# Kernel optimization log

Measured on AMD Instinct MI355X. Metric: run time of the kernel, lower is better.

The kernel has to match this reference:

```python
import jax, jax.numpy as jnp
import numpy as np

B, S, D, H = 2, 2048, 1024, 16
HD = D // H  # 64


def setup_inputs() -> dict:
    key = jax.random.key(0)
    ks = jax.random.split(key, 10)
    s = 1.0 / np.sqrt(D)
    X = jax.random.normal(ks[0], (B, S, D), dtype=jnp.float32)
    # pad the last 256 key positions (nonzero = ignore); causal rows still
    # attend to earlier unpadded keys so no all-masked rows.
    kpm = jnp.broadcast_to((jnp.arange(S) >= S - 256).astype(jnp.int32), (B, S))
    return {
        "X": X,
        "key_padding_mask": kpm,
        "Wq": jax.random.uniform(ks[1], (D, D), jnp.float32, -s, s),
        "bq": jax.random.uniform(ks[2], (D,), jnp.float32, -s, s),
        "Wk": jax.random.uniform(ks[3], (D, D), jnp.float32, -s, s),
        "bk": jax.random.uniform(ks[4], (D,), jnp.float32, -s, s),
        "Wv": jax.random.uniform(ks[5], (D, D), jnp.float32, -s, s),
        "bv": jax.random.uniform(ks[6], (D,), jnp.float32, -s, s),
        "Wo": jax.random.uniform(ks[7], (D, D), jnp.float32, -s, s),
        "bo": jax.random.uniform(ks[8], (D,), jnp.float32, -s, s),
    }


def _mha(X, kpm, Wq, bq, Wk, bk, Wv, bv, Wo, bo):
    b, s, d = X.shape
    def heads(t):  # (b,s,d) -> (b,H,s,hd)
        return t.reshape(b, s, H, HD).transpose(0, 2, 1, 3)
    Q = heads(X @ Wq.T + bq)
    K = heads(X @ Wk.T + bk)
    V = heads(X @ Wv.T + bv)
    scores = jnp.einsum('bhqd,bhkd->bhqk', Q, K) / jnp.sqrt(jnp.float32(HD))
    causal = jnp.triu(jnp.ones((s, s), dtype=bool), k=1)  # True above diag
    scores = jnp.where(causal[None, None], -jnp.inf, scores)
    scores = jnp.where(kpm[:, None, None, :] != 0, -jnp.inf, scores)
    A = jax.nn.softmax(scores, axis=-1)
    out = jnp.einsum('bhqk,bhkd->bhqd', A, V)  # (b,H,s,hd)
    out = out.transpose(0, 2, 1, 3).reshape(b, s, d)
    return out @ Wo.T + bo


def reference(X, key_padding_mask, Wq, bq, Wk, bk, Wv, bv, Wo, bo):
    return _mha(X, key_padding_mask, Wq, bq, Wk, bk, Wv, bv, Wo, bo)
```

## Files before the change

### kernel.cpp

```cpp
#include <hip/hip_runtime.h>
#include <math.h>

#define DEV __device__ __forceinline__

typedef __attribute__((ext_vector_type(4))) float f32x4;
typedef __attribute__((ext_vector_type(8))) __bf16 bf16x8;

static constexpr int Bc = 2, Sc = 2048, Dc = 1024, Hc = 16, HDc = 64;
static constexpr int LDQ = 3 * Dc;
static constexpr float SCL = 0.125f * 1.44269504f;

DEV unsigned short f2b(float f) {
  union { float f; unsigned int u; } c; c.f = f;
  unsigned int u = c.u;
  unsigned int r = (u + 0x7fffu + ((u >> 16) & 1u)) >> 16;
  return (unsigned short)r;
}

DEV void async16(const void* g, void* l) {
  __builtin_amdgcn_global_load_lds(
      (__attribute__((address_space(1))) void*)(void*)g,
      (__attribute__((address_space(3))) void*)l, 16, 0, 0);
}

DEV int swz(int r, int c) { return r * 64 + (c ^ ((r & 7) << 3)); }

__global__ void cvt_x(const float* __restrict__ in,
                      unsigned short* __restrict__ out, int n4) {
  int i = blockIdx.x * blockDim.x + threadIdx.x;
  if (i < n4) {
    const float4 v = reinterpret_cast<const float4*>(in)[i];
    ushort4 o;
    o.x = f2b(v.x); o.y = f2b(v.y); o.z = f2b(v.z); o.w = f2b(v.w);
    reinterpret_cast<ushort4*>(out)[i] = o;
  }
}

__global__ void cvt_w(const float* __restrict__ w0, const float* __restrict__ w1,
                      const float* __restrict__ w2, const float* __restrict__ w3,
                      unsigned short* __restrict__ out) {
  const float* src = blockIdx.y == 0 ? w0
                     : blockIdx.y == 1 ? w1
                     : blockIdx.y == 2 ? w2 : w3;
  const int i = blockIdx.x * blockDim.x + threadIdx.x;
  const float4 v = reinterpret_cast<const float4*>(src)[i];
  ushort4 o;
  o.x = f2b(v.x); o.y = f2b(v.y); o.z = f2b(v.z); o.w = f2b(v.w);
  reinterpret_cast<ushort4*>(out)[(size_t)blockIdx.y * (Dc * Dc / 4) + i] = o;
}

template <typename OUT>
__global__ __launch_bounds__(256, 3) void gemm_bt(
    const unsigned short* __restrict__ A, const unsigned short* __restrict__ Bm,
    const float* __restrict__ b0, const float* __restrict__ b1,
    const float* __restrict__ b2, OUT* __restrict__ C, int M, int K, int ldc) {
  __shared__ unsigned short As[128 * 64];
  __shared__ unsigned short Bs[128 * 64];
  const int tid = threadIdx.x;
  const int wave = tid >> 6, lane = tid & 63;
  const int wr = wave >> 1, wc = wave & 1;
  const int cpx = gridDim.x >> 3;
  const int swzid = (blockIdx.x & 7) * cpx + (blockIdx.x >> 3);
  const int row0 = (swzid & 31) * 128, col0 = (swzid >> 5) * 128;
  const int srow = lane >> 3, scol = (lane & 7) * 8;

  f32x4 acc[4][4];
#pragma unroll
  for (int m = 0; m < 4; ++m)
#pragma unroll
    for (int n = 0; n < 4; ++n) acc[m][n] = {0.f, 0.f, 0.f, 0.f};

  for (int k0 = 0; k0 < K; k0 += 64) {
    __syncthreads();
#pragma unroll
    for (int c = 0; c < 4; ++c) {
      const int rr = (wave * 4 + c) * 8 + srow;
      async16(A + (size_t)(row0 + rr) * K + k0 + scol,
              (char*)As + (wave * 4 + c) * 1024);
      async16(Bm + (size_t)(col0 + rr) * K + k0 + scol,
              (char*)Bs + (wave * 4 + c) * 1024);
    }
    __syncthreads();
#pragma unroll
    for (int ks = 0; ks < 2; ++ks) {
      const int kk = ks * 32 + (lane >> 4) * 8;
      bf16x8 af[4], bfr[4];
#pragma unroll
      for (int m = 0; m < 4; ++m)
        af[m] = *reinterpret_cast<const bf16x8*>(
            &As[(wr * 64 + m * 16 + (lane & 15)) * 64 + kk]);
#pragma unroll
      for (int n = 0; n < 4; ++n)
        bfr[n] = *reinterpret_cast<const bf16x8*>(
            &Bs[(wc * 64 + n * 16 + (lane & 15)) * 64 + kk]);
#pragma unroll
      for (int m = 0; m < 4; ++m)
#pragma unroll
        for (int n = 0; n < 4; ++n)
          acc[m][n] = __builtin_amdgcn_mfma_f32_16x16x32_bf16(af[m], bfr[n],
                                                              acc[m][n], 0, 0, 0);
    }
  }
  const int r4 = (lane >> 4) * 4, cl = lane & 15;
#pragma unroll
  for (int n = 0; n < 4; ++n) {
    const int gc = col0 + wc * 64 + n * 16 + cl;
    const float* bp = gc < Dc ? b0 : (gc < 2 * Dc ? b1 : b2);
    const float bv = bp[gc & (Dc - 1)];
#pragma unroll
    for (int m = 0; m < 4; ++m) {
#pragma unroll
      for (int j = 0; j < 4; ++j) {
        const int gr = row0 + wr * 64 + m * 16 + r4 + j;
        const float v = acc[m][n][j] + bv;
        if constexpr (sizeof(OUT) == 4)
          C[(size_t)gr * ldc + gc] = v;
        else
          C[(size_t)gr * ldc + gc] = (OUT)f2b(v);
      }
    }
  }
}

__global__ __launch_bounds__(256, 4) void attn_fwd(
    const __bf16* __restrict__ Qg, const __bf16* __restrict__ Kg,
    const __bf16* __restrict__ Vg, const int* __restrict__ kpm,
    __bf16* __restrict__ Og) {
  __shared__ __bf16 QP[64 * 64];
  __shared__ __bf16 Ks[2][64 * 64];
  __shared__ __bf16 Vt[2][64 * 64];

  const int L = blockIdx.x;
  const int s = L >> 8, c = L & 255;
  const int u = c >> 5, bh = c & 31;
  const int qb = s * 8 + ((s & 1) ? (7 - u) : u);

  const int b = bh >> 4, h = bh & 15;
  const int q0 = qb * 64;
  const int tid = threadIdx.x, wave = tid >> 6, lane = tid & 63;
  const size_t base = (size_t)b * Sc * LDQ + (size_t)h * HDc;
  const int srow = lane >> 3;
  const int scol = 8 * ((lane & 7) ^ srow);
  const int hi = lane >> 4, cl = lane & 15, r4 = hi * 4;

  const int vk2 = (tid & 31) * 2, vd8 = (tid >> 5) * 8;
  const __bf16* vbase = Vg + base + (size_t)vk2 * LDQ + vd8;
  const int* mbase = kpm + b * Sc;

  union VV { uint4 q; unsigned short u[8]; };

#pragma unroll
  for (int cc = 0; cc < 2; ++cc) {
    const int rr = (wave * 2 + cc) * 8 + srow;
    async16(Qg + base + (size_t)(q0 + rr) * LDQ + scol,
            (char*)QP + (wave * 2 + cc) * 1024);
    async16(Kg + base + (size_t)rr * LDQ + scol,
            (char*)Ks[0] + (wave * 2 + cc) * 1024);
  }
  VV v0, v1;
  v0.q = *reinterpret_cast<const uint4*>(vbase);
  v1.q = *reinterpret_cast<const uint4*>(vbase + LDQ);
  int mki[4];
#pragma unroll
  for (int n = 0; n < 4; ++n) mki[n] = mbase[n * 16 + cl];
  {
    unsigned int* V32 = reinterpret_cast<unsigned int*>(Vt[0]);
#pragma unroll
    for (int i = 0; i < 8; ++i) {
      const int row = vd8 + i;
      V32[row * 32 + ((tid & 31) ^ ((row & 7) << 2))] =
          (unsigned int)v0.u[i] | ((unsigned int)v1.u[i] << 16);
    }
  }
  __syncthreads();

  bf16x8 qf[2];
#pragma unroll
  for (int ks = 0; ks < 2; ++ks)
    qf[ks] = *reinterpret_cast<const bf16x8*>(
        &QP[swz(wave * 16 + cl, ks * 32 + hi * 8)]);
  __bf16* Ps = QP + wave * 1024;

  bf16x8 ones;
#pragma unroll
  for (int i = 0; i < 8; ++i) ones[i] = (__bf16)1.0f;

  f32x4 o[4], lacc;
  float m_[4];
#pragma unroll
  for (int n = 0; n < 4; ++n) o[n] = {0.f, 0.f, 0.f, 0.f};
  lacc = {0.f, 0.f, 0.f, 0.f};
#pragma unroll
  for (int j = 0; j < 4; ++j) m_[j] = -1e30f;

  int pb = 0;
  for (int kb = 0; kb <= qb; ++kb) {
    const bool diag = (kb == qb);
    VV n0, n1;
    int nmk[4];
    if (!diag) {
      const int k1 = (kb + 1) * 64;
#pragma unroll
      for (int cc = 0; cc < 2; ++cc) {
        const int rr = (wave * 2 + cc) * 8 + srow;
        async16(Kg + base + (size_t)(k1 + rr) * LDQ + scol,
                (char*)Ks[pb ^ 1] + (wave * 2 + cc) * 1024);
      }
      n0.q = *reinterpret_cast<const uint4*>(vbase + (size_t)k1 * LDQ);
      n1.q = *reinterpret_cast<const uint4*>(vbase + (size_t)(k1 + 1) * LDQ);
#pragma unroll
      for (int n = 0; n < 4; ++n) nmk[n] = mbase[k1 + n * 16 + cl];
    }

    f32x4 sa[4];
#pragma unroll
    for (int n = 0; n < 4; ++n) sa[n] = {0.f, 0.f, 0.f, 0.f};
    __builtin_amdgcn_s_setprio(1);
#pragma unroll
    for (int ks = 0; ks < 2; ++ks) {
      const int kk = ks * 32 + hi * 8;
#pragma unroll
      for (int n = 0; n < 4; ++n) {
        if (!(diag && n > wave)) {
          const bf16x8 kf = *reinterpret_cast<const bf16x8*>(
              &Ks[pb][swz(n * 16 + cl, kk)]);
          sa[n] = __builtin_amdgcn_mfma_f32_16x16x32_bf16(qf[ks], kf, sa[n],
                                                          0, 0, 0);
        }
      }
    }
    __builtin_amdgcn_s_setprio(0);
    float pm[4] = {-1e30f, -1e30f, -1e30f, -1e30f};
#pragma unroll
    for (int n = 0; n < 4; ++n) {
      const float mf = mki[n] ? -1e30f : 0.0f;
#pragma unroll
      for (int j = 0; j < 4; ++j) {
        float s2 = fmaf(sa[n][j], SCL, mf);
        if (diag && (kb * 64 + n * 16 + cl > q0 + wave * 16 + r4 + j))
          s2 = -1e30f;
        sa[n][j] = s2;
        pm[j] = fmaxf(pm[j], s2);
      }
    }
    const bool ok = (pm[0] - m_[0] <= 8.f) && (pm[1] - m_[1] <= 8.f) &&
                    (pm[2] - m_[2] <= 8.f) && (pm[3] - m_[3] <= 8.f);
    if (!__all(ok)) {
#pragma unroll
      for (int off = 1; off < 16; off <<= 1)
#pragma unroll
        for (int j = 0; j < 4; ++j)
          pm[j] = fmaxf(pm[j], __shfl_xor(pm[j], off, 64));
#pragma unroll
      for (int j = 0; j < 4; ++j) {
        const float mn = fmaxf(m_[j], pm[j]);
        const float sc = __builtin_amdgcn_exp2f(m_[j] - mn);
        m_[j] = mn;
        lacc[j] *= sc;
#pragma unroll
        for (int n = 0; n < 4; ++n) o[n][j] *= sc;
      }
    }
#pragma unroll
    for (int n = 0; n < 4; ++n)
#pragma unroll
      for (int j = 0; j < 4; ++j) {
        const float p = __builtin_amdgcn_exp2f(sa[n][j] - m_[j]);
        Ps[swz(r4 + j, n * 16 + cl)] = (__bf16)p;
      }
    __builtin_amdgcn_s_setprio(1);
#pragma unroll
    for (int ks = 0; ks < 2; ++ks) {
      const int kk = ks * 32 + hi * 8;
      const bf16x8 pf = *reinterpret_cast<const bf16x8*>(&Ps[swz(cl, kk)]);
#pragma unroll
      for (int n = 0; n < 4; ++n) {
        const bf16x8 vf = *reinterpret_cast<const bf16x8*>(
            &Vt[pb][swz(n * 16 + cl, kk)]);
        o[n] = __builtin_amdgcn_mfma_f32_16x16x32_bf16(pf, vf, o[n], 0, 0, 0);
      }
      lacc = __builtin_amdgcn_mfma_f32_16x16x32_bf16(pf, ones, lacc, 0, 0, 0);
    }
    __builtin_amdgcn_s_setprio(0);
    if (!diag) {
      unsigned int* V32 = reinterpret_cast<unsigned int*>(Vt[pb ^ 1]);
#pragma unroll
      for (int i = 0; i < 8; ++i) {
        const int row = vd8 + i;
        V32[row * 32 + ((tid & 31) ^ ((row & 7) << 2))] =
            (unsigned int)n0.u[i] | ((unsigned int)n1.u[i] << 16);
      }
#pragma unroll
      for (int n = 0; n < 4; ++n) mki[n] = nmk[n];
    }
    __syncthreads();
    pb ^= 1;
  }

#pragma unroll
  for (int j = 0; j < 4; ++j) {
    const float inv = 1.f / lacc[j];
#pragma unroll
    for (int n = 0; n < 4; ++n)
      Og[(size_t)(b * Sc + q0 + wave * 16 + r4 + j) * Dc + h * HDc + n * 16 +
         cl] = (__bf16)(o[n][j] * inv);
  }
}

extern "C" void kernel_launch(void* const* d_in, const int* in_sizes, int n_in,
                              void* d_out, int out_size, void* d_ws,
                              size_t ws_size, hipStream_t stream) {
  const float* X = (const float*)d_in[0];
  const int* kpm = (const int*)d_in[1];
  const float* Wq = (const float*)d_in[2];
  const float* bq = (const float*)d_in[3];
  const float* Wk = (const float*)d_in[4];
  const float* bk = (const float*)d_in[5];
  const float* Wv = (const float*)d_in[6];
  const float* bv = (const float*)d_in[7];
  const float* Wo = (const float*)d_in[8];
  const float* bo = (const float*)d_in[9];
  float* out = (float*)d_out;

  char* w = (char*)d_ws;
  unsigned short* Xb = (unsigned short*)(w);
  unsigned short* Wqkvb = (unsigned short*)(w + (8u << 20));
  unsigned short* Wob = (unsigned short*)(w + (14u << 20));
  unsigned short* QKVb = (unsigned short*)(w + (16u << 20));
  unsigned short* Ab = (unsigned short*)(w + (40u << 20));

  const int MD = Bc * Sc;
  cvt_x<<<dim3(MD * Dc / 1024), 256, 0, stream>>>(X, Xb, MD * Dc / 4);
  cvt_w<<<dim3(Dc * Dc / 1024, 4), 256, 0, stream>>>(Wq, Wk, Wv, Wo, Wqkvb);

  gemm_bt<unsigned short><<<dim3(32 * 24), 256, 0, stream>>>(
      Xb, Wqkvb, bq, bk, bv, QKVb, MD, Dc, LDQ);

  attn_fwd<<<dim3(1024), 256, 0, stream>>>(
      (const __bf16*)QKVb, (const __bf16*)QKVb + Dc,
      (const __bf16*)QKVb + 2 * Dc, kpm, (__bf16*)Ab);

  gemm_bt<float><<<dim3(32 * 8), 256, 0, stream>>>(
      Ab, Wob, bo, bo, bo, out, MD, Dc, Dc);
}
```

Measured before the change: 121.6 us.

## Split long causal attention rows across two KV chunks with a combine kernel

Query blocks 8..31 are split into two KV-range chunks, each processed by its own workgroup. Each chunk writes unnormalized bf16 partial outputs plus row max and sum to workspace. A new combine kernel merges the two chunks with log-sum-exp rescaling. The aim is to cut the long tail of the causal workload and even out per-block work, at the cost of an extra launch, partial-result traffic and bf16 rounding of the partials.

```diff
diff --git a/kernel.cpp b/kernel.cpp
--- a/kernel.cpp
+++ b/kernel.cpp
@@ -125,18 +125,36 @@
 __global__ __launch_bounds__(256, 4) void attn_fwd(
     const __bf16* __restrict__ Qg, const __bf16* __restrict__ Kg,
     const __bf16* __restrict__ Vg, const int* __restrict__ kpm,
-    __bf16* __restrict__ Og) {
+    __bf16* __restrict__ Og, __bf16* __restrict__ OP,
+    float* __restrict__ ML) {
   __shared__ __bf16 QP[64 * 64];
   __shared__ __bf16 Ks[2][64 * 64];
   __shared__ __bf16 Vt[2][64 * 64];
 
   const int L = blockIdx.x;
-  const int s = L >> 8, c = L & 255;
-  const int u = c >> 5, bh = c & 31;
-  const int qb = s * 8 + ((s & 1) ? (7 - u) : u);
+  int bh, qb, kb0, kb1, pidx;
+  bool split;
+  if (L < 1536) {
+    qb = 31 - (L >> 6);
+    const int chunk = (L >> 5) & 1;
+    bh = L & 31;
+    const int c0 = (qb + 1) >> 1;
+    kb0 = chunk ? c0 : 0;
+    kb1 = chunk ? qb : c0 - 1;
+    split = true;
+    pidx = (bh * 24 + (qb - 8)) * 2 + chunk;
+  } else {
+    const int b2 = L - 1536;
+    qb = 7 - (b2 >> 5);
+    bh = b2 & 31;
+    kb0 = 0; kb1 = qb;
+    split = false;
+    pidx = 0;
+  }
 
   const int b = bh >> 4, h = bh & 15;
   const int q0 = qb * 64;
+  const int k00 = kb0 * 64;
   const int tid = threadIdx.x, wave = tid >> 6, lane = tid & 63;
   const size_t base = (size_t)b * Sc * LDQ + (size_t)h * HDc;
   const int srow = lane >> 3;
@@ -154,15 +172,15 @@
     const int rr = (wave * 2 + cc) * 8 + srow;
     async16(Qg + base + (size_t)(q0 + rr) * LDQ + scol,
             (char*)QP + (wave * 2 + cc) * 1024);
-    async16(Kg + base + (size_t)rr * LDQ + scol,
+    async16(Kg + base + (size_t)(k00 + rr) * LDQ + scol,
             (char*)Ks[0] + (wave * 2 + cc) * 1024);
   }
   VV v0, v1;
-  v0.q = *reinterpret_cast<const uint4*>(vbase);
-  v1.q = *reinterpret_cast<const uint4*>(vbase + LDQ);
+  v0.q = *reinterpret_cast<const uint4*>(vbase + (size_t)k00 * LDQ);
+  v1.q = *reinterpret_cast<const uint4*>(vbase + (size_t)(k00 + 1) * LDQ);
   int mki[4];
 #pragma unroll
-  for (int n = 0; n < 4; ++n) mki[n] = mbase[n * 16 + cl];
+  for (int n = 0; n < 4; ++n) mki[n] = mbase[k00 + n * 16 + cl];
   {
     unsigned int* V32 = reinterpret_cast<unsigned int*>(Vt[0]);
 #pragma unroll
@@ -194,11 +212,12 @@
   for (int j = 0; j < 4; ++j) m_[j] = -1e30f;
 
   int pb = 0;
-  for (int kb = 0; kb <= qb; ++kb) {
+  for (int kb = kb0; kb <= kb1; ++kb) {
+    const bool last = (kb == kb1);
     const bool diag = (kb == qb);
     VV n0, n1;
     int nmk[4];
-    if (!diag) {
+    if (!last) {
       const int k1 = (kb + 1) * 64;
 #pragma unroll
       for (int cc = 0; cc < 2; ++cc) {
@@ -282,7 +301,7 @@
       lacc = __builtin_amdgcn_mfma_f32_16x16x32_bf16(pf, ones, lacc, 0, 0, 0);
     }
     __builtin_amdgcn_s_setprio(0);
-    if (!diag) {
+    if (!last) {
       unsigned int* V32 = reinterpret_cast<unsigned int*>(Vt[pb ^ 1]);
 #pragma unroll
       for (int i = 0; i < 8; ++i) {
@@ -297,14 +316,64 @@
     pb ^= 1;
   }
 
-#pragma unroll
-  for (int j = 0; j < 4; ++j) {
-    const float inv = 1.f / lacc[j];
-#pragma unroll
-    for (int n = 0; n < 4; ++n)
-      Og[(size_t)(b * Sc + q0 + wave * 16 + r4 + j) * Dc + h * HDc + n * 16 +
-         cl] = (__bf16)(o[n][j] * inv);
-  }
+  if (!split) {
+#pragma unroll
+    for (int j = 0; j < 4; ++j) {
+      const float inv = 1.f / lacc[j];
+#pragma unroll
+      for (int n = 0; n < 4; ++n)
+        Og[(size_t)(b * Sc + q0 + wave * 16 + r4 + j) * Dc + h * HDc + n * 16 +
+           cl] = (__bf16)(o[n][j] * inv);
+    }
+  } else {
+    __bf16* op = OP + (size_t)pidx * 4096;
+    float* ml = ML + (size_t)pidx * 128;
+#pragma unroll
+    for (int j = 0; j < 4; ++j) {
+      const int row = wave * 16 + r4 + j;
+      if (cl == 0) {
+        ml[row * 2 + 0] = m_[j];
+        ml[row * 2 + 1] = lacc[j];
+      }
+#pragma unroll
+      for (int n = 0; n < 4; ++n) op[row * 64 + n * 16 + cl] = (__bf16)o[n][j];
+    }
+  }
+}
+
+__global__ __launch_bounds__(256) void attn_combine(
+    const __bf16* __restrict__ OP, const float* __restrict__ ML,
+    __bf16* __restrict__ Og) {
+  const int qq = blockIdx.x;
+  const int bh = blockIdx.y;
+  const int qb = 8 + qq;
+  const int b = bh >> 4, h = bh & 15;
+  const int t = threadIdx.x;
+  const int row = t >> 2, c0 = (t & 3) * 16;
+  const int p0 = (bh * 24 + qq) * 2;
+  const __bf16* o1 = OP + (size_t)p0 * 4096 + row * 64 + c0;
+  const __bf16* o2 = OP + (size_t)(p0 + 1) * 4096 + row * 64 + c0;
+  const float m1 = ML[(size_t)p0 * 128 + row * 2];
+  const float l1 = ML[(size_t)p0 * 128 + row * 2 + 1];
+  const float m2 = ML[(size_t)(p0 + 1) * 128 + row * 2];
+  const float l2 = ML[(size_t)(p0 + 1) * 128 + row * 2 + 1];
+  const float m = fmaxf(m1, m2);
+  const float s1 = __builtin_amdgcn_exp2f(m1 - m);
+  const float s2 = __builtin_amdgcn_exp2f(m2 - m);
+  const float inv = 1.f / (l1 * s1 + l2 * s2);
+  const bf16x8 a0 = *reinterpret_cast<const bf16x8*>(o1);
+  const bf16x8 a1 = *reinterpret_cast<const bf16x8*>(o1 + 8);
+  const bf16x8 b0 = *reinterpret_cast<const bf16x8*>(o2);
+  const bf16x8 b1 = *reinterpret_cast<const bf16x8*>(o2 + 8);
+  bf16x8 r0, r1;
+#pragma unroll
+  for (int i = 0; i < 8; ++i) {
+    r0[i] = (__bf16)(((float)a0[i] * s1 + (float)b0[i] * s2) * inv);
+    r1[i] = (__bf16)(((float)a1[i] * s1 + (float)b1[i] * s2) * inv);
+  }
+  __bf16* dst = Og + (size_t)(b * Sc + qb * 64 + row) * Dc + h * HDc + c0;
+  *reinterpret_cast<bf16x8*>(dst) = r0;
+  *reinterpret_cast<bf16x8*>(dst + 8) = r1;
 }
 
 extern "C" void kernel_launch(void* const* d_in, const int* in_sizes, int n_in,
@@ -328,6 +397,8 @@
   unsigned short* Wob = (unsigned short*)(w + (14u << 20));
   unsigned short* QKVb = (unsigned short*)(w + (16u << 20));
   unsigned short* Ab = (unsigned short*)(w + (40u << 20));
+  __bf16* OP = (__bf16*)(w);
+  float* ML = (float*)(w + 12'582'912);
 
   const int MD = Bc * Sc;
   cvt_x<<<dim3(MD * Dc / 1024), 256, 0, stream>>>(X, Xb, MD * Dc / 4);
@@ -336,9 +407,10 @@
   gemm_bt<unsigned short><<<dim3(32 * 24), 256, 0, stream>>>(
       Xb, Wqkvb, bq, bk, bv, QKVb, MD, Dc, LDQ);
 
-  attn_fwd<<<dim3(1024), 256, 0, stream>>>(
+  attn_fwd<<<dim3(1792), 256, 0, stream>>>(
       (const __bf16*)QKVb, (const __bf16*)QKVb + Dc,
-      (const __bf16*)QKVb + 2 * Dc, kpm, (__bf16*)Ab);
+      (const __bf16*)QKVb + 2 * Dc, kpm, (__bf16*)Ab, OP, ML);
+  attn_combine<<<dim3(24, 32), 256, 0, stream>>>(OP, ML, (__bf16*)Ab);
 
   gemm_bt<float><<<dim3(32 * 8), 256, 0, stream>>>(
       Ab, Wob, bo, bo, bo, out, MD, Dc, Dc);
```

Result: slower. 129.1 us (+6.2%).

## Use 256x256 double-buffered QKV GEMM and merge conversion kernels

Applied to the files above, without the earlier changes.

Replaces the 128x128 QKV projection GEMM with a new 512-thread kernel using 256x256 tiles, double-buffered async global-to-LDS loads, split barriers and raised wave priority around the MFMA block. The larger tile raises arithmetic intensity and cuts global traffic per FLOP. The X and weight bf16 conversion kernels are merged into one launch to save launch overhead. Risks: only 192 blocks for 256 CUs, so some CUs sit idle and occupancy drops, and the epilogue stores scalar bf16 values.

```diff
diff --git a/kernel.cpp b/kernel.cpp
--- a/kernel.cpp
+++ b/kernel.cpp
@@ -25,28 +25,138 @@
 
 DEV int swz(int r, int c) { return r * 64 + (c ^ ((r & 7) << 3)); }
 
-__global__ void cvt_x(const float* __restrict__ in,
-                      unsigned short* __restrict__ out, int n4) {
-  int i = blockIdx.x * blockDim.x + threadIdx.x;
-  if (i < n4) {
-    const float4 v = reinterpret_cast<const float4*>(in)[i];
-    ushort4 o;
-    o.x = f2b(v.x); o.y = f2b(v.y); o.z = f2b(v.z); o.w = f2b(v.w);
-    reinterpret_cast<ushort4*>(out)[i] = o;
-  }
-}
-
-__global__ void cvt_w(const float* __restrict__ w0, const float* __restrict__ w1,
-                      const float* __restrict__ w2, const float* __restrict__ w3,
-                      unsigned short* __restrict__ out) {
-  const float* src = blockIdx.y == 0 ? w0
-                     : blockIdx.y == 1 ? w1
-                     : blockIdx.y == 2 ? w2 : w3;
+__global__ void cvt_all(const float* __restrict__ X, const float* __restrict__ Wq,
+                        const float* __restrict__ Wk, const float* __restrict__ Wv,
+                        const float* __restrict__ Wo,
+                        unsigned short* __restrict__ Xb,
+                        unsigned short* __restrict__ Wb) {
   const int i = blockIdx.x * blockDim.x + threadIdx.x;
-  const float4 v = reinterpret_cast<const float4*>(src)[i];
-  ushort4 o;
-  o.x = f2b(v.x); o.y = f2b(v.y); o.z = f2b(v.z); o.w = f2b(v.w);
-  reinterpret_cast<ushort4*>(out)[(size_t)blockIdx.y * (Dc * Dc / 4) + i] = o;
+  const float* src;
+  unsigned short* dst;
+  int o;
+  if (i < (1 << 20)) {
+    src = X; o = i; dst = Xb;
+  } else {
+    const int wi = i - (1 << 20);
+    const int m = wi >> 18;
+    src = m == 0 ? Wq : m == 1 ? Wk : m == 2 ? Wv : Wo;
+    o = wi & ((1 << 18) - 1);
+    dst = Wb + (size_t)m * (Dc * Dc);
+  }
+  const float4 v = reinterpret_cast<const float4*>(src)[o];
+  ushort4 u;
+  u.x = f2b(v.x); u.y = f2b(v.y); u.z = f2b(v.z); u.w = f2b(v.w);
+  reinterpret_cast<ushort4*>(dst)[o] = u;
+}
+
+__global__ __launch_bounds__(512, 2) void gemm256(
+    const unsigned short* __restrict__ A, const unsigned short* __restrict__ Bm,
+    const float* __restrict__ b0, const float* __restrict__ b1,
+    const float* __restrict__ b2, unsigned short* __restrict__ C, int K,
+    int ldc) {
+  __shared__ unsigned short As2[2][256 * 64];
+  __shared__ unsigned short Bs2[2][256 * 64];
+  const int tid = threadIdx.x;
+  const int wave = tid >> 6, lane = tid & 63;
+  const int wr = wave >> 2, wc = wave & 3;
+  const int hi = lane >> 4, cl = lane & 15;
+  const int L = K / 64 - 1;
+
+  const int cpx = gridDim.x >> 3;
+  const int id = (blockIdx.x & 7) * cpx + (blockIdx.x >> 3);
+  const int row0 = (id / 12) * 256, col0 = (id % 12) * 256;
+
+  const int trow = tid >> 3;
+  const int scolw = 8 * ((tid & 7) ^ (trow & 7));
+  const unsigned short* Abase = A + (size_t)(row0 + trow) * K + scolw;
+  const unsigned short* Bbase = Bm + (size_t)(col0 + trow) * K + scolw;
+
+  auto stA = [&](int kt, int h) {
+#pragma unroll
+    for (int c = 0; c < 2; ++c)
+      async16(Abase + (size_t)(h * 128 + c * 64) * K + kt * 64,
+              (char*)&As2[kt & 1][(h * 128 + c * 64 + wave * 8) * 64] +
+                  lane * 16);
+  };
+  auto stB = [&](int kt, int h) {
+#pragma unroll
+    for (int c = 0; c < 2; ++c)
+      async16(Bbase + (size_t)(h * 128 + c * 64) * K + kt * 64,
+              (char*)&Bs2[kt & 1][(h * 128 + c * 64 + wave * 8) * 64] +
+                  lane * 16);
+  };
+
+  f32x4 acc[8][4];
+#pragma unroll
+  for (int m = 0; m < 8; ++m)
+#pragma unroll
+    for (int n = 0; n < 4; ++n) acc[m][n] = {0.f, 0.f, 0.f, 0.f};
+
+  stB(0, 0); stB(0, 1); stA(0, 0); stA(0, 1); stB(1, 0); stB(1, 1);
+
+  for (int kt = 0; kt <= L; ++kt) {
+    const int d = kt & 1;
+    if (kt < L)
+      asm volatile("s_waitcnt vmcnt(4)" ::: "memory");
+    else
+      asm volatile("s_waitcnt vmcnt(0)" ::: "memory");
+    __builtin_amdgcn_s_barrier();
+    __builtin_amdgcn_sched_barrier(0);
+
+    bf16x8 bfr[4][2];
+#pragma unroll
+    for (int n = 0; n < 4; ++n)
+#pragma unroll
+      for (int ks = 0; ks < 2; ++ks)
+        bfr[n][ks] = *reinterpret_cast<const bf16x8*>(
+            &Bs2[d][swz(wc * 64 + n * 16 + cl, ks * 32 + hi * 8)]);
+
+#pragma unroll
+    for (int p = 0; p < 4; ++p) {
+      if (p == 2) {
+        __builtin_amdgcn_s_barrier();
+        __builtin_amdgcn_sched_barrier(0);
+      }
+      if (p == 0 && kt < L) stA(kt + 1, 0);
+      if (p == 1 && kt < L) stA(kt + 1, 1);
+      if (p == 2 && kt < L - 1) stB(kt + 2, 0);
+      if (p == 3 && kt < L - 1) stB(kt + 2, 1);
+
+      bf16x8 af[2][2];
+#pragma unroll
+      for (int mf = 0; mf < 2; ++mf)
+#pragma unroll
+        for (int ks = 0; ks < 2; ++ks)
+          af[mf][ks] = *reinterpret_cast<const bf16x8*>(
+              &As2[d][swz(wr * 128 + p * 32 + mf * 16 + cl,
+                          ks * 32 + hi * 8)]);
+      __builtin_amdgcn_s_setprio(1);
+#pragma unroll
+      for (int mf = 0; mf < 2; ++mf)
+#pragma unroll
+        for (int n = 0; n < 4; ++n)
+#pragma unroll
+          for (int ks = 0; ks < 2; ++ks)
+            acc[p * 2 + mf][n] = __builtin_amdgcn_mfma_f32_16x16x32_bf16(
+                af[mf][ks], bfr[n][ks], acc[p * 2 + mf][n], 0, 0, 0);
+      __builtin_amdgcn_s_setprio(0);
+    }
+  }
+
+#pragma unroll
+  for (int n = 0; n < 4; ++n) {
+    const int gc = col0 + wc * 64 + n * 16 + cl;
+    const float* bp = gc < Dc ? b0 : (gc < 2 * Dc ? b1 : b2);
+    const float bv = bp[gc & (Dc - 1)];
+#pragma unroll
+    for (int m = 0; m < 8; ++m) {
+#pragma unroll
+      for (int j = 0; j < 4; ++j) {
+        const int gr = row0 + wr * 128 + m * 16 + hi * 4 + j;
+        C[(size_t)gr * ldc + gc] = f2b(acc[m][n][j] + bv);
+      }
+    }
+  }
 }
 
 template <typename OUT>
@@ -330,11 +440,9 @@
   unsigned short* Ab = (unsigned short*)(w + (40u << 20));
 
   const int MD = Bc * Sc;
-  cvt_x<<<dim3(MD * Dc / 1024), 256, 0, stream>>>(X, Xb, MD * Dc / 4);
-  cvt_w<<<dim3(Dc * Dc / 1024, 4), 256, 0, stream>>>(Wq, Wk, Wv, Wo, Wqkvb);
-
-  gemm_bt<unsigned short><<<dim3(32 * 24), 256, 0, stream>>>(
-      Xb, Wqkvb, bq, bk, bv, QKVb, MD, Dc, LDQ);
+  cvt_all<<<dim3(8192), 256, 0, stream>>>(X, Wq, Wk, Wv, Wo, Xb, Wqkvb);
+
+  gemm256<<<dim3(192), 512, 0, stream>>>(Xb, Wqkvb, bq, bk, bv, QKVb, Dc, LDQ);
 
   attn_fwd<<<dim3(1024), 256, 0, stream>>>(
       (const __bf16*)QKVb, (const __bf16*)QKVb + Dc,
```

After: 125.1 us. +2.9%, slower.

## Transpose QK^T MFMA so each lane owns one query row; fuse converts

Applied to the files above, without the earlier changes.

Swaps the MFMA operands for S=QK^T so each lane holds scores for a single query row, which lets the softmax row max be a scalar per lane reduced with two cross-lane shuffles instead of four-way vectors over 16 lanes. The key padding mask is precomputed once as additive float values, stored temporarily in the output buffer and loaded as f32x4. The X and weight conversion kernels are merged into one launch that also builds the mask. In exchange, the P tile is written to LDS in a transposed pattern and the rescale factor is broadcast with per-row shuffles, which may add LDS bank conflicts and shuffle cost.

```diff
diff --git a/kernel.cpp b/kernel.cpp
--- a/kernel.cpp
+++ b/kernel.cpp
@@ -25,28 +25,34 @@
 
 DEV int swz(int r, int c) { return r * 64 + (c ^ ((r & 7) << 3)); }
 
-__global__ void cvt_x(const float* __restrict__ in,
-                      unsigned short* __restrict__ out, int n4) {
-  int i = blockIdx.x * blockDim.x + threadIdx.x;
-  if (i < n4) {
-    const float4 v = reinterpret_cast<const float4*>(in)[i];
-    ushort4 o;
-    o.x = f2b(v.x); o.y = f2b(v.y); o.z = f2b(v.z); o.w = f2b(v.w);
-    reinterpret_cast<ushort4*>(out)[i] = o;
-  }
-}
-
-__global__ void cvt_w(const float* __restrict__ w0, const float* __restrict__ w1,
-                      const float* __restrict__ w2, const float* __restrict__ w3,
-                      unsigned short* __restrict__ out) {
-  const float* src = blockIdx.y == 0 ? w0
-                     : blockIdx.y == 1 ? w1
-                     : blockIdx.y == 2 ? w2 : w3;
+__global__ void cvt_all(const float* __restrict__ X, const float* __restrict__ Wq,
+                        const float* __restrict__ Wk, const float* __restrict__ Wv,
+                        const float* __restrict__ Wo, const int* __restrict__ kpm,
+                        unsigned short* __restrict__ Xb,
+                        unsigned short* __restrict__ Wb,
+                        float* __restrict__ mfl) {
   const int i = blockIdx.x * blockDim.x + threadIdx.x;
-  const float4 v = reinterpret_cast<const float4*>(src)[i];
-  ushort4 o;
-  o.x = f2b(v.x); o.y = f2b(v.y); o.z = f2b(v.z); o.w = f2b(v.w);
-  reinterpret_cast<ushort4*>(out)[(size_t)blockIdx.y * (Dc * Dc / 4) + i] = o;
+  if (i >= (1 << 21)) {
+    const int mi = i - (1 << 21);
+    if (mi < Bc * Sc) mfl[mi] = kpm[mi] ? -1e30f : 0.0f;
+    return;
+  }
+  const float* src;
+  unsigned short* dst;
+  int o;
+  if (i < (1 << 20)) {
+    src = X; o = i; dst = Xb;
+  } else {
+    const int wi = i - (1 << 20);
+    const int m = wi >> 18;
+    src = m == 0 ? Wq : m == 1 ? Wk : m == 2 ? Wv : Wo;
+    o = wi & ((1 << 18) - 1);
+    dst = Wb + (size_t)m * (Dc * Dc);
+  }
+  const float4 v = reinterpret_cast<const float4*>(src)[o];
+  ushort4 u;
+  u.x = f2b(v.x); u.y = f2b(v.y); u.z = f2b(v.z); u.w = f2b(v.w);
+  reinterpret_cast<ushort4*>(dst)[o] = u;
 }
 
 template <typename OUT>
@@ -124,7 +130,7 @@
 
 __global__ __launch_bounds__(256, 4) void attn_fwd(
     const __bf16* __restrict__ Qg, const __bf16* __restrict__ Kg,
-    const __bf16* __restrict__ Vg, const int* __restrict__ kpm,
+    const __bf16* __restrict__ Vg, const float* __restrict__ mfl,
     __bf16* __restrict__ Og) {
   __shared__ __bf16 QP[64 * 64];
   __shared__ __bf16 Ks[2][64 * 64];
@@ -142,10 +148,11 @@
   const int srow = lane >> 3;
   const int scol = 8 * ((lane & 7) ^ srow);
   const int hi = lane >> 4, cl = lane & 15, r4 = hi * 4;
+  const int myq = q0 + wave * 16 + cl;
 
   const int vk2 = (tid & 31) * 2, vd8 = (tid >> 5) * 8;
   const __bf16* vbase = Vg + base + (size_t)vk2 * LDQ + vd8;
-  const int* mbase = kpm + b * Sc;
+  const float* mbase = mfl + b * Sc;
 
   union VV { uint4 q; unsigned short u[8]; };
 
@@ -160,9 +167,10 @@
   VV v0, v1;
   v0.q = *reinterpret_cast<const uint4*>(vbase);
   v1.q = *reinterpret_cast<const uint4*>(vbase + LDQ);
-  int mki[4];
-#pragma unroll
-  for (int n = 0; n < 4; ++n) mki[n] = mbase[n * 16 + cl];
+  f32x4 mk[4];
+#pragma unroll
+  for (int n = 0; n < 4; ++n)
+    mk[n] = *reinterpret_cast<const f32x4*>(&mbase[n * 16 + hi * 4]);
   {
     unsigned int* V32 = reinterpret_cast<unsigned int*>(Vt[0]);
 #pragma unroll
@@ -186,18 +194,16 @@
   for (int i = 0; i < 8; ++i) ones[i] = (__bf16)1.0f;
 
   f32x4 o[4], lacc;
-  float m_[4];
+  float m_ = -1e30f;
 #pragma unroll
   for (int n = 0; n < 4; ++n) o[n] = {0.f, 0.f, 0.f, 0.f};
   lacc = {0.f, 0.f, 0.f, 0.f};
-#pragma unroll
-  for (int j = 0; j < 4; ++j) m_[j] = -1e30f;
 
   int pb = 0;
   for (int kb = 0; kb <= qb; ++kb) {
     const bool diag = (kb == qb);
     VV n0, n1;
-    int nmk[4];
+    f32x4 nmk[4];
     if (!diag) {
       const int k1 = (kb + 1) * 64;
 #pragma unroll
@@ -209,7 +215,8 @@
       n0.q = *reinterpret_cast<const uint4*>(vbase + (size_t)k1 * LDQ);
       n1.q = *reinterpret_cast<const uint4*>(vbase + (size_t)(k1 + 1) * LDQ);
 #pragma unroll
-      for (int n = 0; n < 4; ++n) nmk[n] = mbase[k1 + n * 16 + cl];
+      for (int n = 0; n < 4; ++n)
+        nmk[n] = *reinterpret_cast<const f32x4*>(&mbase[k1 + n * 16 + hi * 4]);
     }
 
     f32x4 sa[4];
@@ -224,49 +231,43 @@
         if (!(diag && n > wave)) {
           const bf16x8 kf = *reinterpret_cast<const bf16x8*>(
               &Ks[pb][swz(n * 16 + cl, kk)]);
-          sa[n] = __builtin_amdgcn_mfma_f32_16x16x32_bf16(qf[ks], kf, sa[n],
+          sa[n] = __builtin_amdgcn_mfma_f32_16x16x32_bf16(kf, qf[ks], sa[n],
                                                           0, 0, 0);
         }
       }
     }
     __builtin_amdgcn_s_setprio(0);
-    float pm[4] = {-1e30f, -1e30f, -1e30f, -1e30f};
+    float pm = -1e30f;
 #pragma unroll
     for (int n = 0; n < 4; ++n) {
-      const float mf = mki[n] ? -1e30f : 0.0f;
 #pragma unroll
       for (int j = 0; j < 4; ++j) {
-        float s2 = fmaf(sa[n][j], SCL, mf);
-        if (diag && (kb * 64 + n * 16 + cl > q0 + wave * 16 + r4 + j))
-          s2 = -1e30f;
+        float s2 = fmaf(sa[n][j], SCL, mk[n][j]);
+        if (diag && (kb * 64 + n * 16 + hi * 4 + j > myq)) s2 = -1e30f;
         sa[n][j] = s2;
-        pm[j] = fmaxf(pm[j], s2);
-      }
-    }
-    const bool ok = (pm[0] - m_[0] <= 8.f) && (pm[1] - m_[1] <= 8.f) &&
-                    (pm[2] - m_[2] <= 8.f) && (pm[3] - m_[3] <= 8.f);
-    if (!__all(ok)) {
-#pragma unroll
-      for (int off = 1; off < 16; off <<= 1)
-#pragma unroll
-        for (int j = 0; j < 4; ++j)
-          pm[j] = fmaxf(pm[j], __shfl_xor(pm[j], off, 64));
+        pm = fmaxf(pm, s2);
+      }
+    }
+    if (!__all(pm - m_ <= 8.f)) {
+      pm = fmaxf(pm, __shfl_xor(pm, 16, 64));
+      pm = fmaxf(pm, __shfl_xor(pm, 32, 64));
+      const float mn = fmaxf(m_, pm);
+      const float sc = __builtin_amdgcn_exp2f(m_ - mn);
+      m_ = mn;
 #pragma unroll
       for (int j = 0; j < 4; ++j) {
-        const float mn = fmaxf(m_[j], pm[j]);
-        const float sc = __builtin_amdgcn_exp2f(m_[j] - mn);
-        m_[j] = mn;
-        lacc[j] *= sc;
-#pragma unroll
-        for (int n = 0; n < 4; ++n) o[n][j] *= sc;
+        const float scj = __shfl(sc, r4 + j, 64);
+        lacc[j] *= scj;
+#pragma unroll
+        for (int n = 0; n < 4; ++n) o[n][j] *= scj;
       }
     }
 #pragma unroll
     for (int n = 0; n < 4; ++n)
 #pragma unroll
       for (int j = 0; j < 4; ++j) {
-        const float p = __builtin_amdgcn_exp2f(sa[n][j] - m_[j]);
-        Ps[swz(r4 + j, n * 16 + cl)] = (__bf16)p;
+        const float p = __builtin_amdgcn_exp2f(sa[n][j] - m_);
+        Ps[swz(cl, n * 16 + hi * 4 + j)] = (__bf16)p;
       }
     __builtin_amdgcn_s_setprio(1);
 #pragma unroll
@@ -291,7 +292,7 @@
             (unsigned int)n0.u[i] | ((unsigned int)n1.u[i] << 16);
       }
 #pragma unroll
-      for (int n = 0; n < 4; ++n) mki[n] = nmk[n];
+      for (int n = 0; n < 4; ++n) mk[n] = nmk[n];
     }
     __syncthreads();
     pb ^= 1;
@@ -328,17 +329,18 @@
   unsigned short* Wob = (unsigned short*)(w + (14u << 20));
   unsigned short* QKVb = (unsigned short*)(w + (16u << 20));
   unsigned short* Ab = (unsigned short*)(w + (40u << 20));
+  float* mfl = out;
 
   const int MD = Bc * Sc;
-  cvt_x<<<dim3(MD * Dc / 1024), 256, 0, stream>>>(X, Xb, MD * Dc / 4);
-  cvt_w<<<dim3(Dc * Dc / 1024, 4), 256, 0, stream>>>(Wq, Wk, Wv, Wo, Wqkvb);
+  cvt_all<<<dim3(8208), 256, 0, stream>>>(X, Wq, Wk, Wv, Wo, kpm, Xb, Wqkvb,
+                                          mfl);
 
   gemm_bt<unsigned short><<<dim3(32 * 24), 256, 0, stream>>>(
       Xb, Wqkvb, bq, bk, bv, QKVb, MD, Dc, LDQ);
 
   attn_fwd<<<dim3(1024), 256, 0, stream>>>(
       (const __bf16*)QKVb, (const __bf16*)QKVb + Dc,
-      (const __bf16*)QKVb + 2 * Dc, kpm, (__bf16*)Ab);
+      (const __bf16*)QKVb + 2 * Dc, mfl, (__bf16*)Ab);
 
   gemm_bt<float><<<dim3(32 * 8), 256, 0, stream>>>(
       Ab, Wob, bo, bo, bo, out, MD, Dc, Dc);
```

New measurement: 131.4 us. 8.0% more time.
